# Kernel optimization log

Hardware: AMD Instinct MI355X
Metric: run time of the kernel (lower is better)

Reference implementation:

```python
import jax, jax.numpy as jnp
import numpy as np

B, N, D = 4, 2048, 2048
HEADS, KV_HEADS = 16, 4
DH = D // HEADS            # 128 per-head dim
KV_RATIO = HEADS // KV_HEADS
MAX_LEN, MAX_BSZ = 2048, 4
EPS = 1.1920929e-07        # torch.finfo(float32).eps (RMSNorm default eps=None)


def _rot_tables(n, d, base=10000.0):
    thetas = base ** (-jnp.arange(0, d, 2, dtype=jnp.float32) / d)   # [d/2]
    ang = jnp.arange(n, dtype=jnp.float32)[:, None] * thetas[None, :]
    cos = jnp.repeat(jnp.cos(ang), 2, axis=-1)   # [n, d] interleaved pairs
    sin = jnp.repeat(jnp.sin(ang), 2, axis=-1)
    return cos, sin


def _rotate_half_inverted(x):
    x1 = x[..., ::2]
    x2 = x[..., 1::2]
    return jnp.stack([-x2, x1], axis=-1).reshape(x.shape)


def _apply_rotation(x, end, start=0):
    cos, sin = _rot_tables(MAX_LEN, DH)
    return x * cos[start:end] + _rotate_half_inverted(x) * sin[start:end]


def setup_inputs() -> dict:
    key = jax.random.key(0)
    ks = jax.random.split(key, 4)
    s = 0.02
    return {
        "x": jax.random.normal(ks[0], (B, N, D), jnp.float32),
        "norm_w": jnp.ones((D,), jnp.float32),
        "qw": jax.random.normal(ks[1], (HEADS * DH, D), jnp.float32) * s,
        "qb": jnp.zeros((HEADS * DH,), jnp.float32),
        "kvw": jax.random.normal(ks[2], (2 * DH * KV_HEADS, D), jnp.float32) * s,
        "kvb": jnp.zeros((2 * DH * KV_HEADS,), jnp.float32),
        "wow": jax.random.normal(ks[3], (D, HEADS * DH), jnp.float32) * s,
        "wob": jnp.zeros((D,), jnp.float32),
        "kv_cache": jnp.zeros((MAX_BSZ, MAX_LEN, 2 * DH * KV_HEADS), jnp.float32),
        "pos": 0,
    }


def reference(x, norm_w, qw, qb, kvw, kvb, wow, wob, kv_cache, pos):
    b, n, d = x.shape
    t = pos + n  # total cached length
    # RMSNorm
    xn = x * jax.lax.rsqrt(jnp.mean(x * x, axis=-1, keepdims=True) + EPS) * norm_w
    # Q projection -> [b, heads, n, dh]
    q = (xn @ qw.T + qb).reshape(b, n, HEADS, DH).transpose(0, 2, 1, 3)
    # KV projection + cache write/read
    kv = xn @ kvw.T + kvb                                  # [b, n, 2*dh*kv_heads]
    cache = jax.lax.dynamic_update_slice(kv_cache, kv, (0, pos, 0))
    kvf = cache[:b, :t].reshape(b, t, KV_HEADS, 2 * DH).transpose(0, 2, 1, 3)
    kvf = jnp.repeat(kvf, KV_RATIO, axis=1)                # GQA expand -> [b, heads, t, 2dh]
    k, v = kvf[..., :DH], kvf[..., DH:]
    # RoPE (interleaved-pair variant)
    q = _apply_rotation(q, t, pos)
    k = _apply_rotation(k, t, 0)
    # Attention (decoder causal)
    attn = jnp.einsum("bhqd,bhkd->bhqk", q, k) / jnp.sqrt(jnp.float32(DH))
    if n > 1:
        mask = jnp.triu(jnp.ones((n, t), bool), k=1 + pos)
        attn = jnp.where(mask, -jnp.inf, attn)
    attn = jax.nn.softmax(attn, axis=-1)
    o = jnp.einsum("bhqk,bhkd->bhqd", attn, v).transpose(0, 2, 1, 3).reshape(b, n, HEADS * DH)
    return o @ wow.T + wob
```

## Files before the change

### kernel.cpp

```cpp
#include <hip/hip_runtime.h>
#include <hip/hip_bf16.h>

typedef unsigned short u16;
typedef unsigned int u32;
typedef __attribute__((ext_vector_type(4))) float f32x4;
typedef __attribute__((ext_vector_type(8))) short s16x8;

#define B_ 4
#define N_ 2048
#define D_ 2048
#define HEADS_ 16
#define KVH_ 4
#define DH_ 128
#define KVD_ 1024
#define M_ 8192
#define QSCALE2_ 0.12753257518622628f

__device__ __forceinline__ u16 f2bf(float f) {
  u32 u = __builtin_bit_cast(u32, f);
  return (u16)((u + 0x7FFFu + ((u >> 16) & 1u)) >> 16);
}

__device__ __forceinline__ float fexp2(float x) {
#if __has_builtin(__builtin_amdgcn_exp2f)
  return __builtin_amdgcn_exp2f(x);
#else
  return exp2f(x);
#endif
}

__device__ __forceinline__ void gload_lds16(const void* g, void* l) {
  __builtin_amdgcn_global_load_lds(
      (const __attribute__((address_space(1))) u32*)g,
      (__attribute__((address_space(3))) u32*)l, 16, 0, 0);
}

__global__ __launch_bounds__(256)
void rope_tab_k(float* __restrict__ cost, float* __restrict__ sint)
{
  const int idx = blockIdx.x * 256 + threadIdx.x;
  const int p = idx >> 6, i = idx & 63;
  const float theta = expf(-(float)i * 0.015625f * 9.210340371976184f);
  float s, c;
  sincosf((float)p * theta, &s, &c);
  cost[idx] = c;
  sint[idx] = s;
}

__global__ __launch_bounds__(256)
void cvt_bf16_k(const float* __restrict__ s, u16* __restrict__ d, int n)
{
  const int i = (blockIdx.x * 256 + threadIdx.x) * 8;
  if (i >= n) return;
  const f32x4 a = *(const f32x4*)(s + i);
  const f32x4 b = *(const f32x4*)(s + i + 4);
  s16x8 o;
  #pragma unroll
  for (int j = 0; j < 4; ++j) { o[j] = (short)f2bf(a[j]); o[4 + j] = (short)f2bf(b[j]); }
  *(s16x8*)(d + i) = o;
}

__global__ __launch_bounds__(256)
void rmsnorm_k(const float* __restrict__ x, const float* __restrict__ w, u16* __restrict__ xn)
{
  const int row = blockIdx.x, t = threadIdx.x;
  const float* xr = x + (size_t)row * D_;
  const f32x4 a = *(const f32x4*)(xr + t * 8);
  const f32x4 b = *(const f32x4*)(xr + t * 8 + 4);
  float ss = a[0]*a[0] + a[1]*a[1] + a[2]*a[2] + a[3]*a[3]
           + b[0]*b[0] + b[1]*b[1] + b[2]*b[2] + b[3]*b[3];
  #pragma unroll
  for (int off = 32; off >= 1; off >>= 1) ss += __shfl_xor(ss, off);
  __shared__ float wss[4];
  if ((t & 63) == 0) wss[t >> 6] = ss;
  __syncthreads();
  const float tot = wss[0] + wss[1] + wss[2] + wss[3];
  const float rs = rsqrtf(tot * (1.0f / D_) + 1.1920929e-07f);
  s16x8 o;
  #pragma unroll
  for (int j = 0; j < 4; ++j) {
    o[j]     = (short)f2bf(a[j] * rs * w[t * 8 + j]);
    o[4 + j] = (short)f2bf(b[j] * rs * w[t * 8 + 4 + j]);
  }
  *(s16x8*)(xn + (size_t)row * D_ + t * 8) = o;
}

template<int EPI>
__global__ __launch_bounds__(512, 2)
void gemm_p(const u16* __restrict__ A, const u16* __restrict__ Bw,
            void* __restrict__ Cv, void* __restrict__ Cv2,
            const float* __restrict__ bias, const float* __restrict__ bias2,
            const float* __restrict__ cos_t, const float* __restrict__ sin_t)
{
  __shared__ __align__(16) u16 As[2][8192];
  __shared__ __align__(16) u16 Bs[2][4096];
  const int t = threadIdx.x, w = t >> 6, l = t & 63;
  const int g = l >> 4, lr = l & 15;
  const int wm = w >> 2, wn = w & 3;

  const int nbx = gridDim.x;
  const int nb = nbx * gridDim.y;
  const int flat = blockIdx.y * nbx + blockIdx.x;
  const int swz = (flat & 7) * (nb >> 3) + (flat >> 3);
  const int row0 = (swz / nbx) * 256, col0 = (swz % nbx) * 128;

  const int NT = 64;

  const int srow = w * 16 + (l >> 2);
  const int scol = (l & 3) * 8;
  const u16* gA = A + (size_t)(row0 + srow) * 2048 + scol;
  const u16* gB = Bw + (size_t)(col0 + srow) * 2048 + scol;

  f32x4 acc[8][2] = {};

  auto stage_tile = [&](int kt2, int pb) {
    gload_lds16(gA + (size_t)kt2 * 32, &As[pb][(w * 16) * 32]);
    gload_lds16(gA + (size_t)128 * 2048 + kt2 * 32, &As[pb][(128 + w * 16) * 32]);
    gload_lds16(gB + (size_t)kt2 * 32, &Bs[pb][(w * 16) * 32]);
  };

  stage_tile(0, 0);

  for (int kt = 0; kt < NT; ++kt) {
    const int p = kt & 1;
    if (kt + 1 < NT) {
      stage_tile(kt + 1, p ^ 1);
      asm volatile("s_waitcnt vmcnt(3)" ::: "memory");
    } else {
      asm volatile("s_waitcnt vmcnt(0)" ::: "memory");
    }
    __builtin_amdgcn_s_barrier();

    s16x8 bf[2], af[8];
    #pragma unroll
    for (int nf = 0; nf < 2; ++nf)
      bf[nf] = *(const s16x8*)(&Bs[p][(wn * 32 + nf * 16 + lr) * 32 + g * 8]);
    #pragma unroll
    for (int mf = 0; mf < 8; ++mf)
      af[mf] = *(const s16x8*)(&As[p][(wm * 128 + mf * 16 + lr) * 32 + g * 8]);

    __builtin_amdgcn_s_setprio(1);
    #pragma unroll
    for (int mf = 0; mf < 8; ++mf)
      #pragma unroll
      for (int nf = 0; nf < 2; ++nf)
        acc[mf][nf] = __builtin_amdgcn_mfma_f32_16x16x32_bf16(af[mf], bf[nf], acc[mf][nf], 0, 0, 0);
    __builtin_amdgcn_s_setprio(0);
    __builtin_amdgcn_sched_barrier(0);
    __builtin_amdgcn_s_barrier();
  }

  #pragma unroll
  for (int mf = 0; mf < 8; ++mf) {
    #pragma unroll
    for (int nf = 0; nf < 2; ++nf) {
      const int cc = col0 + wn * 32 + nf * 16 + lr;
      const float bv = (EPI == 4 && cc >= 2048) ? bias2[cc - 2048] : bias[cc];
      #pragma unroll
      for (int j = 0; j < 4; ++j) {
        const int rr = row0 + wm * 128 + mf * 16 + g * 4 + j;
        float v = acc[mf][nf][j] + bv;
        if (EPI == 0) {
          ((float*)Cv)[(size_t)rr * 2048 + cc] = v;
        } else {
          const int pos = rr & (N_ - 1);
          const float pv = __shfl_xor(v, 1);
          if (cc < 2048) {
            const int d = cc & (DH_ - 1);
            const float c = cos_t[pos * 64 + (d >> 1)];
            const float s = sin_t[pos * 64 + (d >> 1)];
            const float o = (cc & 1) ? fmaf(v, c, pv * s) : fmaf(v, c, -pv * s);
            ((u16*)Cv)[(size_t)rr * 2048 + cc] = f2bf(o);
          } else {
            const int ccc = cc - 2048;
            const int dm = ccc & 255;
            float o = v;
            if (dm < DH_) {
              const float c = cos_t[pos * 64 + (dm >> 1)];
              const float s = sin_t[pos * 64 + (dm >> 1)];
              o = (dm & 1) ? fmaf(v, c, pv * s) : fmaf(v, c, -pv * s);
            }
            ((u16*)Cv2)[(size_t)rr * 1024 + ccc] = f2bf(o);
          }
        }
      }
    }
  }
}

__global__ __launch_bounds__(256)
void vtrans_k(const u16* __restrict__ kvb, u16* __restrict__ vt)
{
  __shared__ u16 tile[64][65];
  const int z = blockIdx.z, b = z >> 2, kh = z & 3;
  const int p0 = blockIdx.x * 64, d0 = blockIdx.y * 64;
  const int t = threadIdx.x;
  #pragma unroll
  for (int r = 0; r < 2; ++r) {
    const int pl = r * 32 + (t >> 3), dl = (t & 7) * 8;
    const s16x8 v = *(const s16x8*)(kvb + (size_t)(b * N_ + p0 + pl) * KVD_ + kh * 256 + 128 + d0 + dl);
    #pragma unroll
    for (int jj = 0; jj < 8; ++jj) tile[pl][dl + jj] = (u16)v[jj];
  }
  __syncthreads();
  #pragma unroll
  for (int r = 0; r < 2; ++r) {
    const int dl = r * 32 + (t >> 3), pl = (t & 7) * 8;
    s16x8 o;
    #pragma unroll
    for (int jj = 0; jj < 8; ++jj) o[jj] = (short)tile[pl + jj][dl];
    *(s16x8*)(vt + ((size_t)(z * DH_ + d0 + dl)) * N_ + p0 + pl) = o;
  }
}

__global__ __launch_bounds__(512, 2)
void attn_k(const u16* __restrict__ q, const u16* __restrict__ kvb,
            const u16* __restrict__ vt, u16* __restrict__ out)
{
  const int fi = blockIdx.x, h = blockIdx.y, b = blockIdx.z;
  const int kh = h >> 2;
  const int t = threadIdx.x, w = t >> 6, lane = t & 63;
  const int g = lane >> 4, lr = lane & 15;

  __shared__ __align__(16) u16 Ks[2][64 * 128];
  __shared__ __align__(16) u16 Vs[2][128 * 64];
  __shared__ __align__(16) u16 Ps[8][16 * 64];

  const int kc = 2 * w;
  const int kr0 = kc * 4 + (lane >> 4);
  const int ksw0 = (lane & 15) ^ (kr0 & 7);
  const int kr1 = kr0 + 4;
  const int ksw1 = (lane & 15) ^ (kr1 & 7);
  const int vd0 = kc * 8 + (lane >> 3);
  const int vsw0 = (lane & 7) ^ (vd0 & 7);
  const int vd1 = vd0 + 8;
  const int vsw1 = (lane & 7) ^ (vd1 & 7);

  const u16* kbase = kvb + (size_t)b * (N_ * KVD_) + kh * 256;
  const u16* vbase = vt + (size_t)((b * KVH_ + kh) * DH_) * N_;

  int cur = 0;

  auto issue = [&](int kt, int buf) {
    gload_lds16(kbase + (size_t)(kt * 64 + kr0) * KVD_ + ksw0 * 8, &Ks[buf][kc * 512]);
    gload_lds16(kbase + (size_t)(kt * 64 + kr1) * KVD_ + ksw1 * 8, &Ks[buf][(kc + 1) * 512]);
    gload_lds16(vbase + (size_t)vd0 * N_ + kt * 64 + vsw0 * 8, &Vs[buf][kc * 512]);
    gload_lds16(vbase + (size_t)vd1 * N_ + kt * 64 + vsw1 * 8, &Vs[buf][(kc + 1) * 512]);
  };

  auto run_qtile = [&](int qi, int nkt, bool chain) {
    const int qrow0 = qi * 128 + w * 16;
    const int td = qrow0 >> 6;
    s16x8 qf[4];
    {
      const u16* qp = q + (size_t)(b * N_ + qrow0 + lr) * D_ + h * DH_;
      #pragma unroll
      for (int ks = 0; ks < 4; ++ks) qf[ks] = *(const s16x8*)(qp + ks * 32 + g * 8);
    }
    f32x4 o_acc[8] = {};
    float m_j[4], l_j[4];
    #pragma unroll
    for (int j = 0; j < 4; ++j) { m_j[j] = -1e30f; l_j[j] = 0.0f; }

    for (int kt = 0; kt < nkt; ++kt) {
      __syncthreads();
      if (kt + 1 < nkt)      issue(kt + 1, cur ^ 1);
      else if (chain)        issue(0, cur ^ 1);

      if (kt <= td) {
        const u16* Kc = &Ks[cur][0];
        const u16* Vc = &Vs[cur][0];

        f32x4 sf[4] = {};
        __builtin_amdgcn_s_setprio(1);
        #pragma unroll
        for (int ks = 0; ks < 4; ++ks) {
          #pragma unroll
          for (int kvf = 0; kvf < 4; ++kvf) {
            const int kvr = kvf * 16 + lr;
            const int ba = (kvr * 256 + ks * 64 + g * 16) ^ ((kvr & 7) << 4);
            const s16x8 kf = *(const s16x8*)((const char*)Kc + ba);
            sf[kvf] = __builtin_amdgcn_mfma_f32_16x16x32_bf16(qf[ks], kf, sf[kvf], 0, 0, 0);
          }
        }
        __builtin_amdgcn_s_setprio(0);

        const bool need_mask = (kt == td);
        float pmax[4];
        #pragma unroll
        for (int j = 0; j < 4; ++j) {
          float mx = -1e30f;
          #pragma unroll
          for (int kvf = 0; kvf < 4; ++kvf) {
            float sv = sf[kvf][j] * QSCALE2_;
            if (need_mask) {
              const int kj = kt * 64 + kvf * 16 + lr;
              const int qi_row = qrow0 + g * 4 + j;
              if (kj > qi_row) sv = -1e30f;
            }
            sf[kvf][j] = sv;
            mx = fmaxf(mx, sv);
          }
          mx = fmaxf(mx, __shfl_xor(mx, 1));
          mx = fmaxf(mx, __shfl_xor(mx, 2));
          mx = fmaxf(mx, __shfl_xor(mx, 4));
          mx = fmaxf(mx, __shfl_xor(mx, 8));
          pmax[j] = mx;
        }

        const float needv = fmaxf(fmaxf(pmax[0] - m_j[0], pmax[1] - m_j[1]),
                                  fmaxf(pmax[2] - m_j[2], pmax[3] - m_j[3]));
        if (__any(needv > 8.0f)) {
          #pragma unroll
          for (int j = 0; j < 4; ++j) {
            const float mn = fmaxf(m_j[j], pmax[j]);
            const float pf = fexp2(m_j[j] - mn);
            m_j[j] = mn;
            l_j[j] *= pf;
            #pragma unroll
            for (int df = 0; df < 8; ++df) o_acc[df][j] *= pf;
          }
        }

        #pragma unroll
        for (int j = 0; j < 4; ++j) {
          float lacc = 0.0f;
          #pragma unroll
          for (int kvf = 0; kvf < 4; ++kvf) {
            const float p = fexp2(sf[kvf][j] - m_j[j]);
            lacc += p;
            const int rq = g * 4 + j, ck = kvf * 16 + lr;
            const int ba = (rq * 128 + ck * 2) ^ ((rq & 7) << 4);
            *(u16*)((char*)&Ps[w][0] + ba) = (u16)(__builtin_bit_cast(u32, p) >> 16);
          }
          l_j[j] += lacc;
        }

        __builtin_amdgcn_s_setprio(1);
        #pragma unroll
        for (int kk = 0; kk < 2; ++kk) {
          const int bap = (lr * 128 + kk * 64 + g * 16) ^ ((lr & 7) << 4);
          const s16x8 pf = *(const s16x8*)((const char*)&Ps[w][0] + bap);
          #pragma unroll
          for (int df = 0; df < 8; ++df) {
            const int dd = df * 16 + lr;
            const int bav = (dd * 128 + kk * 64 + g * 16) ^ ((dd & 7) << 4);
            const s16x8 vf = *(const s16x8*)((const char*)Vc + bav);
            o_acc[df] = __builtin_amdgcn_mfma_f32_16x16x32_bf16(pf, vf, o_acc[df], 0, 0, 0);
          }
        }
        __builtin_amdgcn_s_setprio(0);
      }
      cur ^= 1;
    }

    float inv_l[4];
    #pragma unroll
    for (int j = 0; j < 4; ++j) {
      float s4 = l_j[j];
      s4 += __shfl_xor(s4, 1);
      s4 += __shfl_xor(s4, 2);
      s4 += __shfl_xor(s4, 4);
      s4 += __shfl_xor(s4, 8);
      inv_l[j] = 1.0f / s4;
    }
    u16* op = out + (size_t)(b * N_ + qrow0) * D_ + h * DH_;
    #pragma unroll
    for (int df = 0; df < 8; ++df)
      #pragma unroll
      for (int j = 0; j < 4; ++j)
        op[(size_t)(g * 4 + j) * D_ + df * 16 + lr] = f2bf(o_acc[df][j] * inv_l[j]);
  };

  const int qlo = fi, qhi = 15 - fi;
  issue(0, 0);
  run_qtile(qlo, 2 * qlo + 2, true);
  run_qtile(qhi, 2 * qhi + 2, false);
}

extern "C" void kernel_launch(void* const* d_in, const int* in_sizes, int n_in,
                              void* d_out, int out_size, void* d_ws, size_t ws_size,
                              hipStream_t stream) {
  const float* x      = (const float*)d_in[0];
  const float* normw  = (const float*)d_in[1];
  const float* qw     = (const float*)d_in[2];
  const float* qbias  = (const float*)d_in[3];
  const float* kvw    = (const float*)d_in[4];
  const float* kvbias = (const float*)d_in[5];
  const float* wow    = (const float*)d_in[6];
  const float* wob    = (const float*)d_in[7];
  float* out = (float*)d_out;

  char* ws = (char*)d_ws;
  u16* xn    = (u16*)(ws + 0);
  u16* dq    = (u16*)(ws + 33554432);
  u16* dkv   = (u16*)(ws + 67108864);
  u16* dvt   = (u16*)(ws + 83886080);
  u16* wqkv  = (u16*)(ws + 92274688);
  u16* wowb  = (u16*)(ws + 104857600);
  float* cost = (float*)(ws + 113246208);
  float* sint = (float*)(ws + 113770496);

  rope_tab_k<<<512, 256, 0, stream>>>(cost, sint);
  cvt_bf16_k<<<2048, 256, 0, stream>>>(qw, wqkv, 2048 * 2048);
  cvt_bf16_k<<<1024, 256, 0, stream>>>(kvw, wqkv + 2048 * 2048, 1024 * 2048);
  cvt_bf16_k<<<2048, 256, 0, stream>>>(wow, wowb, 2048 * 2048);
  rmsnorm_k<<<8192, 256, 0, stream>>>(x, normw, xn);
  gemm_p<4><<<dim3(24, 32), 512, 0, stream>>>(xn, wqkv, (void*)dq, (void*)dkv,
                                              qbias, kvbias, cost, sint);
  vtrans_k<<<dim3(32, 2, 16), 256, 0, stream>>>(dkv, dvt);
  attn_k<<<dim3(8, 16, 4), 512, 0, stream>>>(dq, dkv, dvt, xn);
  gemm_p<0><<<dim3(16, 32), 512, 0, stream>>>(xn, wowb, (void*)out, nullptr,
                                              wob, nullptr, nullptr, nullptr);
}
```

Measured before the change: 423.1 us.

## Single-buffer V tile, reload Q per tile, and add Ps swizzle bit

V is now loaded into a single LDS buffer within the same iteration rather than double-buffered ahead, with an explicit vmcnt wait before the PV MFMA. The goal is to cut LDS use and let more blocks fit per CU. Q fragments are re-read from global memory each live iteration instead of being held in registers for the whole tile, which lowers register pressure. The P-tile swizzle gains a higher XOR bit to reduce LDS bank conflicts. In exchange, V load latency is exposed within each iteration and Q is reloaded repeatedly.

```diff
diff --git a/kernel.cpp b/kernel.cpp
--- a/kernel.cpp
+++ b/kernel.cpp
@@ -223,40 +223,36 @@
   const int g = lane >> 4, lr = lane & 15;
 
   __shared__ __align__(16) u16 Ks[2][64 * 128];
-  __shared__ __align__(16) u16 Vs[2][128 * 64];
+  __shared__ __align__(16) u16 Vs[128 * 64];
   __shared__ __align__(16) u16 Ps[8][16 * 64];
-
-  const int kc = 2 * w;
-  const int kr0 = kc * 4 + (lane >> 4);
-  const int ksw0 = (lane & 15) ^ (kr0 & 7);
-  const int kr1 = kr0 + 4;
-  const int ksw1 = (lane & 15) ^ (kr1 & 7);
-  const int vd0 = kc * 8 + (lane >> 3);
-  const int vsw0 = (lane & 7) ^ (vd0 & 7);
-  const int vd1 = vd0 + 8;
-  const int vsw1 = (lane & 7) ^ (vd1 & 7);
 
   const u16* kbase = kvb + (size_t)b * (N_ * KVD_) + kh * 256;
   const u16* vbase = vt + (size_t)((b * KVH_ + kh) * DH_) * N_;
 
-  int cur = 0;
-
-  auto issue = [&](int kt, int buf) {
+  auto issueK = [&](int kt, int buf) {
+    const int kc = 2 * w;
+    const int kr0 = kc * 4 + (lane >> 4);
+    const int ksw0 = (lane & 15) ^ (kr0 & 7);
+    const int kr1 = kr0 + 4;
+    const int ksw1 = (lane & 15) ^ (kr1 & 7);
     gload_lds16(kbase + (size_t)(kt * 64 + kr0) * KVD_ + ksw0 * 8, &Ks[buf][kc * 512]);
     gload_lds16(kbase + (size_t)(kt * 64 + kr1) * KVD_ + ksw1 * 8, &Ks[buf][(kc + 1) * 512]);
-    gload_lds16(vbase + (size_t)vd0 * N_ + kt * 64 + vsw0 * 8, &Vs[buf][kc * 512]);
-    gload_lds16(vbase + (size_t)vd1 * N_ + kt * 64 + vsw1 * 8, &Vs[buf][(kc + 1) * 512]);
   };
+  auto issueV = [&](int kt) {
+    const int kc = 2 * w;
+    const int vd0 = kc * 8 + (lane >> 3);
+    const int vsw0 = (lane & 7) ^ (vd0 & 7);
+    const int vd1 = vd0 + 8;
+    const int vsw1 = (lane & 7) ^ (vd1 & 7);
+    gload_lds16(vbase + (size_t)vd0 * N_ + kt * 64 + vsw0 * 8, &Vs[kc * 512]);
+    gload_lds16(vbase + (size_t)vd1 * N_ + kt * 64 + vsw1 * 8, &Vs[(kc + 1) * 512]);
+  };
+
+  int cur = 0;
 
   auto run_qtile = [&](int qi, int nkt, bool chain) {
     const int qrow0 = qi * 128 + w * 16;
     const int td = qrow0 >> 6;
-    s16x8 qf[4];
-    {
-      const u16* qp = q + (size_t)(b * N_ + qrow0 + lr) * D_ + h * DH_;
-      #pragma unroll
-      for (int ks = 0; ks < 4; ++ks) qf[ks] = *(const s16x8*)(qp + ks * 32 + g * 8);
-    }
     f32x4 o_acc[8] = {};
     float m_j[4], l_j[4];
     #pragma unroll
@@ -264,12 +260,22 @@
 
     for (int kt = 0; kt < nkt; ++kt) {
       __syncthreads();
-      if (kt + 1 < nkt)      issue(kt + 1, cur ^ 1);
-      else if (chain)        issue(0, cur ^ 1);
-
-      if (kt <= td) {
+      const bool live = (kt <= td);
+      const bool havek = (kt + 1 < nkt) || chain;
+
+      s16x8 qf[4];
+      if (live) {
+        int zoff; asm volatile("s_mov_b32 %0, 0" : "=s"(zoff));
+        const u16* qp = q + (size_t)(b * N_ + qrow0 + lr) * D_ + h * DH_ + zoff;
+        #pragma unroll
+        for (int ks = 0; ks < 4; ++ks) qf[ks] = *(const s16x8*)(qp + ks * 32 + g * 8);
+      }
+      issueV(kt);
+      if (kt + 1 < nkt)      issueK(kt + 1, cur ^ 1);
+      else if (chain)        issueK(0, cur ^ 1);
+
+      if (live) {
         const u16* Kc = &Ks[cur][0];
-        const u16* Vc = &Vs[cur][0];
 
         f32x4 sf[4] = {};
         __builtin_amdgcn_s_setprio(1);
@@ -330,22 +336,25 @@
             const float p = fexp2(sf[kvf][j] - m_j[j]);
             lacc += p;
             const int rq = g * 4 + j, ck = kvf * 16 + lr;
-            const int ba = (rq * 128 + ck * 2) ^ ((rq & 7) << 4);
+            const int ba = rq * 128 + ((ck * 2) ^ ((rq & 7) << 4) ^ ((rq & 8) << 2));
             *(u16*)((char*)&Ps[w][0] + ba) = (u16)(__builtin_bit_cast(u32, p) >> 16);
           }
           l_j[j] += lacc;
         }
+
+        if (havek) asm volatile("s_waitcnt vmcnt(2)" ::: "memory");
+        else       asm volatile("s_waitcnt vmcnt(0)" ::: "memory");
 
         __builtin_amdgcn_s_setprio(1);
         #pragma unroll
         for (int kk = 0; kk < 2; ++kk) {
-          const int bap = (lr * 128 + kk * 64 + g * 16) ^ ((lr & 7) << 4);
+          const int bap = lr * 128 + ((kk * 64 + g * 16) ^ ((lr & 7) << 4) ^ ((lr & 8) << 2));
           const s16x8 pf = *(const s16x8*)((const char*)&Ps[w][0] + bap);
           #pragma unroll
           for (int df = 0; df < 8; ++df) {
             const int dd = df * 16 + lr;
             const int bav = (dd * 128 + kk * 64 + g * 16) ^ ((dd & 7) << 4);
-            const s16x8 vf = *(const s16x8*)((const char*)Vc + bav);
+            const s16x8 vf = *(const s16x8*)((const char*)Vs + bav);
             o_acc[df] = __builtin_amdgcn_mfma_f32_16x16x32_bf16(pf, vf, o_acc[df], 0, 0, 0);
           }
         }
@@ -373,7 +382,7 @@
   };
 
   const int qlo = fi, qhi = 15 - fi;
-  issue(0, 0);
+  issueK(0, 0);
   run_qtile(qlo, 2 * qlo + 2, true);
   run_qtile(qhi, 2 * qhi + 2, false);
 }
```

After: 453.3 us. +7.2%, slower.

## Shrink attention tiles to 64 query rows and 32-key blocks, drop paired tiles

Applied to the files above, without the earlier changes.

The attention kernel now uses 256-thread blocks, each covering one 64-row query tile, with 32-key K/V tiles. It replaces the old scheme where each 512-thread block processed a paired light and heavy 128-row tile. Blocks are launched heaviest-first (qi = 31 - blockIdx.x) to balance the causal load, and the K/V swizzles and P buffer padding are redone for the smaller tiles. This means more, smaller blocks and less LDS per block, so occupancy should rise. In exchange, each loaded K/V tile is reused by fewer queries and there are more barrier iterations per unit of work.

```diff
diff --git a/kernel.cpp b/kernel.cpp
--- a/kernel.cpp
+++ b/kernel.cpp
@@ -213,169 +213,156 @@
   }
 }
 
-__global__ __launch_bounds__(512, 2)
+__global__ __launch_bounds__(256, 3)
 void attn_k(const u16* __restrict__ q, const u16* __restrict__ kvb,
             const u16* __restrict__ vt, u16* __restrict__ out)
 {
-  const int fi = blockIdx.x, h = blockIdx.y, b = blockIdx.z;
+  const int qi = 31 - blockIdx.x, h = blockIdx.y, b = blockIdx.z;
   const int kh = h >> 2;
   const int t = threadIdx.x, w = t >> 6, lane = t & 63;
   const int g = lane >> 4, lr = lane & 15;
 
-  __shared__ __align__(16) u16 Ks[2][64 * 128];
-  __shared__ __align__(16) u16 Vs[2][128 * 64];
-  __shared__ __align__(16) u16 Ps[8][16 * 64];
-
-  const int kc = 2 * w;
-  const int kr0 = kc * 4 + (lane >> 4);
-  const int ksw0 = (lane & 15) ^ (kr0 & 7);
-  const int kr1 = kr0 + 4;
-  const int ksw1 = (lane & 15) ^ (kr1 & 7);
-  const int vd0 = kc * 8 + (lane >> 3);
-  const int vsw0 = (lane & 7) ^ (vd0 & 7);
-  const int vd1 = vd0 + 8;
-  const int vsw1 = (lane & 7) ^ (vd1 & 7);
+  __shared__ __align__(16) u16 Ks[2][32 * 128];
+  __shared__ __align__(16) u16 Vs[2][128 * 32];
+  __shared__ __align__(16) u16 Ps[4][16 * 40];
 
   const u16* kbase = kvb + (size_t)b * (N_ * KVD_) + kh * 256;
   const u16* vbase = vt + (size_t)((b * KVH_ + kh) * DH_) * N_;
 
+  auto issue = [&](int kt, int buf) {
+    #pragma unroll
+    for (int i = 0; i < 2; ++i) {
+      const int c = 2 * w + i;
+      const int kr = 4 * c + (lane >> 4);
+      const int ksw = (lane & 15) ^ (kr & 15);
+      gload_lds16(kbase + (size_t)(kt * 32 + kr) * KVD_ + ksw * 8, &Ks[buf][c * 512]);
+      const int vr = 16 * c + (lane >> 2);
+      const int vsw = (lane & 3) ^ (vr & 3);
+      gload_lds16(vbase + (size_t)vr * N_ + kt * 32 + vsw * 8, &Vs[buf][c * 512]);
+    }
+  };
+
+  const int qrow0 = qi * 64 + w * 16;
+  const int td = (qrow0 + 15) >> 5;
+  const int nkt = 2 * qi + 2;
+
+  s16x8 qf[4];
+  {
+    const u16* qp = q + (size_t)(b * N_ + qrow0 + lr) * D_ + h * DH_;
+    #pragma unroll
+    for (int ks = 0; ks < 4; ++ks) qf[ks] = *(const s16x8*)(qp + ks * 32 + g * 8);
+  }
+  f32x4 o_acc[8] = {};
+  float m_j[4], l_j[4];
+  #pragma unroll
+  for (int j = 0; j < 4; ++j) { m_j[j] = -1e30f; l_j[j] = 0.0f; }
+
+  issue(0, 0);
   int cur = 0;
 
-  auto issue = [&](int kt, int buf) {
-    gload_lds16(kbase + (size_t)(kt * 64 + kr0) * KVD_ + ksw0 * 8, &Ks[buf][kc * 512]);
-    gload_lds16(kbase + (size_t)(kt * 64 + kr1) * KVD_ + ksw1 * 8, &Ks[buf][(kc + 1) * 512]);
-    gload_lds16(vbase + (size_t)vd0 * N_ + kt * 64 + vsw0 * 8, &Vs[buf][kc * 512]);
-    gload_lds16(vbase + (size_t)vd1 * N_ + kt * 64 + vsw1 * 8, &Vs[buf][(kc + 1) * 512]);
-  };
-
-  auto run_qtile = [&](int qi, int nkt, bool chain) {
-    const int qrow0 = qi * 128 + w * 16;
-    const int td = qrow0 >> 6;
-    s16x8 qf[4];
-    {
-      const u16* qp = q + (size_t)(b * N_ + qrow0 + lr) * D_ + h * DH_;
-      #pragma unroll
-      for (int ks = 0; ks < 4; ++ks) qf[ks] = *(const s16x8*)(qp + ks * 32 + g * 8);
-    }
-    f32x4 o_acc[8] = {};
-    float m_j[4], l_j[4];
-    #pragma unroll
-    for (int j = 0; j < 4; ++j) { m_j[j] = -1e30f; l_j[j] = 0.0f; }
-
-    for (int kt = 0; kt < nkt; ++kt) {
-      __syncthreads();
-      if (kt + 1 < nkt)      issue(kt + 1, cur ^ 1);
-      else if (chain)        issue(0, cur ^ 1);
-
-      if (kt <= td) {
-        const u16* Kc = &Ks[cur][0];
-        const u16* Vc = &Vs[cur][0];
-
-        f32x4 sf[4] = {};
-        __builtin_amdgcn_s_setprio(1);
+  for (int kt = 0; kt < nkt; ++kt) {
+    __syncthreads();
+    if (kt + 1 < nkt) issue(kt + 1, cur ^ 1);
+
+    if (kt <= td) {
+      const u16* Kc = &Ks[cur][0];
+      const u16* Vc = &Vs[cur][0];
+
+      f32x4 sf[2] = {};
+      __builtin_amdgcn_s_setprio(1);
+      #pragma unroll
+      for (int ks = 0; ks < 4; ++ks) {
         #pragma unroll
-        for (int ks = 0; ks < 4; ++ks) {
-          #pragma unroll
-          for (int kvf = 0; kvf < 4; ++kvf) {
-            const int kvr = kvf * 16 + lr;
-            const int ba = (kvr * 256 + ks * 64 + g * 16) ^ ((kvr & 7) << 4);
-            const s16x8 kf = *(const s16x8*)((const char*)Kc + ba);
-            sf[kvf] = __builtin_amdgcn_mfma_f32_16x16x32_bf16(qf[ks], kf, sf[kvf], 0, 0, 0);
+        for (int kvf = 0; kvf < 2; ++kvf) {
+          const int kvr = kvf * 16 + lr;
+          const int ba = kvr * 256 + ((ks * 64 + g * 16) ^ ((kvr & 15) << 4));
+          const s16x8 kf = *(const s16x8*)((const char*)Kc + ba);
+          sf[kvf] = __builtin_amdgcn_mfma_f32_16x16x32_bf16(qf[ks], kf, sf[kvf], 0, 0, 0);
+        }
+      }
+      __builtin_amdgcn_s_setprio(0);
+
+      const bool need_mask = (kt == td);
+      float pmax[4];
+      #pragma unroll
+      for (int j = 0; j < 4; ++j) {
+        float mx = -1e30f;
+        #pragma unroll
+        for (int kvf = 0; kvf < 2; ++kvf) {
+          float sv = sf[kvf][j] * QSCALE2_;
+          if (need_mask) {
+            const int kj = kt * 32 + kvf * 16 + lr;
+            const int qi_row = qrow0 + g * 4 + j;
+            if (kj > qi_row) sv = -1e30f;
           }
+          sf[kvf][j] = sv;
+          mx = fmaxf(mx, sv);
         }
-        __builtin_amdgcn_s_setprio(0);
-
-        const bool need_mask = (kt == td);
-        float pmax[4];
+        mx = fmaxf(mx, __shfl_xor(mx, 1));
+        mx = fmaxf(mx, __shfl_xor(mx, 2));
+        mx = fmaxf(mx, __shfl_xor(mx, 4));
+        mx = fmaxf(mx, __shfl_xor(mx, 8));
+        pmax[j] = mx;
+      }
+
+      const float needv = fmaxf(fmaxf(pmax[0] - m_j[0], pmax[1] - m_j[1]),
+                                fmaxf(pmax[2] - m_j[2], pmax[3] - m_j[3]));
+      if (__any(needv > 8.0f)) {
         #pragma unroll
         for (int j = 0; j < 4; ++j) {
-          float mx = -1e30f;
+          const float mn = fmaxf(m_j[j], pmax[j]);
+          const float pf = fexp2(m_j[j] - mn);
+          m_j[j] = mn;
+          l_j[j] *= pf;
           #pragma unroll
-          for (int kvf = 0; kvf < 4; ++kvf) {
-            float sv = sf[kvf][j] * QSCALE2_;
-            if (need_mask) {
-              const int kj = kt * 64 + kvf * 16 + lr;
-              const int qi_row = qrow0 + g * 4 + j;
-              if (kj > qi_row) sv = -1e30f;
-            }
-            sf[kvf][j] = sv;
-            mx = fmaxf(mx, sv);
-          }
-          mx = fmaxf(mx, __shfl_xor(mx, 1));
-          mx = fmaxf(mx, __shfl_xor(mx, 2));
-          mx = fmaxf(mx, __shfl_xor(mx, 4));
-          mx = fmaxf(mx, __shfl_xor(mx, 8));
-          pmax[j] = mx;
+          for (int df = 0; df < 8; ++df) o_acc[df][j] *= pf;
         }
-
-        const float needv = fmaxf(fmaxf(pmax[0] - m_j[0], pmax[1] - m_j[1]),
-                                  fmaxf(pmax[2] - m_j[2], pmax[3] - m_j[3]));
-        if (__any(needv > 8.0f)) {
-          #pragma unroll
-          for (int j = 0; j < 4; ++j) {
-            const float mn = fmaxf(m_j[j], pmax[j]);
-            const float pf = fexp2(m_j[j] - mn);
-            m_j[j] = mn;
-            l_j[j] *= pf;
-            #pragma unroll
-            for (int df = 0; df < 8; ++df) o_acc[df][j] *= pf;
-          }
+      }
+
+      #pragma unroll
+      for (int j = 0; j < 4; ++j) {
+        float lacc = 0.0f;
+        #pragma unroll
+        for (int kvf = 0; kvf < 2; ++kvf) {
+          const float p = fexp2(sf[kvf][j] - m_j[j]);
+          lacc += p;
+          const int rq = g * 4 + j, ck = kvf * 16 + lr;
+          *(u16*)((char*)&Ps[w][0] + rq * 80 + ck * 2) =
+              (u16)(__builtin_bit_cast(u32, p) >> 16);
         }
-
-        #pragma unroll
-        for (int j = 0; j < 4; ++j) {
-          float lacc = 0.0f;
-          #pragma unroll
-          for (int kvf = 0; kvf < 4; ++kvf) {
-            const float p = fexp2(sf[kvf][j] - m_j[j]);
-            lacc += p;
-            const int rq = g * 4 + j, ck = kvf * 16 + lr;
-            const int ba = (rq * 128 + ck * 2) ^ ((rq & 7) << 4);
-            *(u16*)((char*)&Ps[w][0] + ba) = (u16)(__builtin_bit_cast(u32, p) >> 16);
-          }
-          l_j[j] += lacc;
-        }
-
-        __builtin_amdgcn_s_setprio(1);
-        #pragma unroll
-        for (int kk = 0; kk < 2; ++kk) {
-          const int bap = (lr * 128 + kk * 64 + g * 16) ^ ((lr & 7) << 4);
-          const s16x8 pf = *(const s16x8*)((const char*)&Ps[w][0] + bap);
-          #pragma unroll
-          for (int df = 0; df < 8; ++df) {
-            const int dd = df * 16 + lr;
-            const int bav = (dd * 128 + kk * 64 + g * 16) ^ ((dd & 7) << 4);
-            const s16x8 vf = *(const s16x8*)((const char*)Vc + bav);
-            o_acc[df] = __builtin_amdgcn_mfma_f32_16x16x32_bf16(pf, vf, o_acc[df], 0, 0, 0);
-          }
-        }
-        __builtin_amdgcn_s_setprio(0);
-      }
-      cur ^= 1;
+        l_j[j] += lacc;
+      }
+
+      const s16x8 pf = *(const s16x8*)((const char*)&Ps[w][0] + lr * 80 + g * 16);
+      __builtin_amdgcn_s_setprio(1);
+      #pragma unroll
+      for (int df = 0; df < 8; ++df) {
+        const int dd = df * 16 + lr;
+        const int bav = dd * 64 + ((g * 16) ^ ((dd & 3) << 4));
+        const s16x8 vf = *(const s16x8*)((const char*)Vc + bav);
+        o_acc[df] = __builtin_amdgcn_mfma_f32_16x16x32_bf16(pf, vf, o_acc[df], 0, 0, 0);
+      }
+      __builtin_amdgcn_s_setprio(0);
     }
-
-    float inv_l[4];
-    #pragma unroll
-    for (int j = 0; j < 4; ++j) {
-      float s4 = l_j[j];
-      s4 += __shfl_xor(s4, 1);
-      s4 += __shfl_xor(s4, 2);
-      s4 += __shfl_xor(s4, 4);
-      s4 += __shfl_xor(s4, 8);
-      inv_l[j] = 1.0f / s4;
-    }
-    u16* op = out + (size_t)(b * N_ + qrow0) * D_ + h * DH_;
-    #pragma unroll
-    for (int df = 0; df < 8; ++df)
-      #pragma unroll
-      for (int j = 0; j < 4; ++j)
-        op[(size_t)(g * 4 + j) * D_ + df * 16 + lr] = f2bf(o_acc[df][j] * inv_l[j]);
-  };
-
-  const int qlo = fi, qhi = 15 - fi;
-  issue(0, 0);
-  run_qtile(qlo, 2 * qlo + 2, true);
-  run_qtile(qhi, 2 * qhi + 2, false);
+    cur ^= 1;
+  }
+
+  float inv_l[4];
+  #pragma unroll
+  for (int j = 0; j < 4; ++j) {
+    float s4 = l_j[j];
+    s4 += __shfl_xor(s4, 1);
+    s4 += __shfl_xor(s4, 2);
+    s4 += __shfl_xor(s4, 4);
+    s4 += __shfl_xor(s4, 8);
+    inv_l[j] = 1.0f / s4;
+  }
+  u16* op = out + (size_t)(b * N_ + qrow0) * D_ + h * DH_;
+  #pragma unroll
+  for (int df = 0; df < 8; ++df)
+    #pragma unroll
+    for (int j = 0; j < 4; ++j)
+      op[(size_t)(g * 4 + j) * D_ + df * 16 + lr] = f2bf(o_acc[df][j] * inv_l[j]);
 }
 
 extern "C" void kernel_launch(void* const* d_in, const int* in_sizes, int n_in,
@@ -409,7 +396,7 @@
   gemm_p<4><<<dim3(24, 32), 512, 0, stream>>>(xn, wqkv, (void*)dq, (void*)dkv,
                                               qbias, kvbias, cost, sint);
   vtrans_k<<<dim3(32, 2, 16), 256, 0, stream>>>(dkv, dvt);
-  attn_k<<<dim3(8, 16, 4), 512, 0, stream>>>(dq, dkv, dvt, xn);
+  attn_k<<<dim3(32, 16, 4), 256, 0, stream>>>(dq, dkv, dvt, xn);
   gemm_p<0><<<dim3(16, 32), 512, 0, stream>>>(xn, wowb, (void*)out, nullptr,
                                               wob, nullptr, nullptr, nullptr);
 }
```

Result: slower. 538.3 us (+27.2%).

## Triple-buffer K/V tiles in attention with a single fused loop over both q-tiles

Applied to the files above, without the earlier changes.

Replaces the double-buffered K/V LDS staging with a three-stage ring, issuing loads two tiles ahead and waiting with explicit vmcnt counts before each barrier. The two per-block q-tiles are merged into one flat loop, so the prefetch continues across the tile boundary. The point is to hide more global-load latency behind MFMA work. In exchange LDS use rises, and launch bounds drop to one block per CU, which lowers occupancy.

```diff
diff --git a/kernel.cpp b/kernel.cpp
--- a/kernel.cpp
+++ b/kernel.cpp
@@ -213,7 +213,7 @@
   }
 }
 
-__global__ __launch_bounds__(512, 2)
+__global__ __launch_bounds__(512, 1)
 void attn_k(const u16* __restrict__ q, const u16* __restrict__ kvb,
             const u16* __restrict__ vt, u16* __restrict__ out)
 {
@@ -222,8 +222,8 @@
   const int t = threadIdx.x, w = t >> 6, lane = t & 63;
   const int g = lane >> 4, lr = lane & 15;
 
-  __shared__ __align__(16) u16 Ks[2][64 * 128];
-  __shared__ __align__(16) u16 Vs[2][128 * 64];
+  __shared__ __align__(16) u16 Ks[3][64 * 128];
+  __shared__ __align__(16) u16 Vs[3][128 * 64];
   __shared__ __align__(16) u16 Ps[8][16 * 64];
 
   const int kc = 2 * w;
@@ -239,8 +239,6 @@
   const u16* kbase = kvb + (size_t)b * (N_ * KVD_) + kh * 256;
   const u16* vbase = vt + (size_t)((b * KVH_ + kh) * DH_) * N_;
 
-  int cur = 0;
-
   auto issue = [&](int kt, int buf) {
     gload_lds16(kbase + (size_t)(kt * 64 + kr0) * KVD_ + ksw0 * 8, &Ks[buf][kc * 512]);
     gload_lds16(kbase + (size_t)(kt * 64 + kr1) * KVD_ + ksw1 * 8, &Ks[buf][(kc + 1) * 512]);
@@ -248,112 +246,25 @@
     gload_lds16(vbase + (size_t)vd1 * N_ + kt * 64 + vsw1 * 8, &Vs[buf][(kc + 1) * 512]);
   };
 
-  auto run_qtile = [&](int qi, int nkt, bool chain) {
-    const int qrow0 = qi * 128 + w * 16;
-    const int td = qrow0 >> 6;
-    s16x8 qf[4];
-    {
-      const u16* qp = q + (size_t)(b * N_ + qrow0 + lr) * D_ + h * DH_;
-      #pragma unroll
-      for (int ks = 0; ks < 4; ++ks) qf[ks] = *(const s16x8*)(qp + ks * 32 + g * 8);
-    }
-    f32x4 o_acc[8] = {};
-    float m_j[4], l_j[4];
-    #pragma unroll
-    for (int j = 0; j < 4; ++j) { m_j[j] = -1e30f; l_j[j] = 0.0f; }
-
-    for (int kt = 0; kt < nkt; ++kt) {
-      __syncthreads();
-      if (kt + 1 < nkt)      issue(kt + 1, cur ^ 1);
-      else if (chain)        issue(0, cur ^ 1);
-
-      if (kt <= td) {
-        const u16* Kc = &Ks[cur][0];
-        const u16* Vc = &Vs[cur][0];
-
-        f32x4 sf[4] = {};
-        __builtin_amdgcn_s_setprio(1);
-        #pragma unroll
-        for (int ks = 0; ks < 4; ++ks) {
-          #pragma unroll
-          for (int kvf = 0; kvf < 4; ++kvf) {
-            const int kvr = kvf * 16 + lr;
-            const int ba = (kvr * 256 + ks * 64 + g * 16) ^ ((kvr & 7) << 4);
-            const s16x8 kf = *(const s16x8*)((const char*)Kc + ba);
-            sf[kvf] = __builtin_amdgcn_mfma_f32_16x16x32_bf16(qf[ks], kf, sf[kvf], 0, 0, 0);
-          }
-        }
-        __builtin_amdgcn_s_setprio(0);
-
-        const bool need_mask = (kt == td);
-        float pmax[4];
-        #pragma unroll
-        for (int j = 0; j < 4; ++j) {
-          float mx = -1e30f;
-          #pragma unroll
-          for (int kvf = 0; kvf < 4; ++kvf) {
-            float sv = sf[kvf][j] * QSCALE2_;
-            if (need_mask) {
-              const int kj = kt * 64 + kvf * 16 + lr;
-              const int qi_row = qrow0 + g * 4 + j;
-              if (kj > qi_row) sv = -1e30f;
-            }
-            sf[kvf][j] = sv;
-            mx = fmaxf(mx, sv);
-          }
-          mx = fmaxf(mx, __shfl_xor(mx, 1));
-          mx = fmaxf(mx, __shfl_xor(mx, 2));
-          mx = fmaxf(mx, __shfl_xor(mx, 4));
-          mx = fmaxf(mx, __shfl_xor(mx, 8));
-          pmax[j] = mx;
-        }
-
-        const float needv = fmaxf(fmaxf(pmax[0] - m_j[0], pmax[1] - m_j[1]),
-                                  fmaxf(pmax[2] - m_j[2], pmax[3] - m_j[3]));
-        if (__any(needv > 8.0f)) {
-          #pragma unroll
-          for (int j = 0; j < 4; ++j) {
-            const float mn = fmaxf(m_j[j], pmax[j]);
-            const float pf = fexp2(m_j[j] - mn);
-            m_j[j] = mn;
-            l_j[j] *= pf;
-            #pragma unroll
-            for (int df = 0; df < 8; ++df) o_acc[df][j] *= pf;
-          }
-        }
-
-        #pragma unroll
-        for (int j = 0; j < 4; ++j) {
-          float lacc = 0.0f;
-          #pragma unroll
-          for (int kvf = 0; kvf < 4; ++kvf) {
-            const float p = fexp2(sf[kvf][j] - m_j[j]);
-            lacc += p;
-            const int rq = g * 4 + j, ck = kvf * 16 + lr;
-            const int ba = (rq * 128 + ck * 2) ^ ((rq & 7) << 4);
-            *(u16*)((char*)&Ps[w][0] + ba) = (u16)(__builtin_bit_cast(u32, p) >> 16);
-          }
-          l_j[j] += lacc;
-        }
-
-        __builtin_amdgcn_s_setprio(1);
-        #pragma unroll
-        for (int kk = 0; kk < 2; ++kk) {
-          const int bap = (lr * 128 + kk * 64 + g * 16) ^ ((lr & 7) << 4);
-          const s16x8 pf = *(const s16x8*)((const char*)&Ps[w][0] + bap);
-          #pragma unroll
-          for (int df = 0; df < 8; ++df) {
-            const int dd = df * 16 + lr;
-            const int bav = (dd * 128 + kk * 64 + g * 16) ^ ((dd & 7) << 4);
-            const s16x8 vf = *(const s16x8*)((const char*)Vc + bav);
-            o_acc[df] = __builtin_amdgcn_mfma_f32_16x16x32_bf16(pf, vf, o_acc[df], 0, 0, 0);
-          }
-        }
-        __builtin_amdgcn_s_setprio(0);
-      }
-      cur ^= 1;
-    }
-
+  const int qlo = fi, qhi = 15 - fi;
+  const int nkt0 = 2 * qlo + 2;
+  const int ntot = nkt0 + 2 * qhi + 2;
+
+  int qrow0 = qlo * 128 + w * 16;
+  int td = qrow0 >> 6;
+
+  s16x8 qf[4];
+  {
+    const u16* qp = q + (size_t)(b * N_ + qrow0 + lr) * D_ + h * DH_;
+    #pragma unroll
+    for (int ks = 0; ks < 4; ++ks) qf[ks] = *(const s16x8*)(qp + ks * 32 + g * 8);
+  }
+  f32x4 o_acc[8] = {};
+  float m_j[4], l_j[4];
+  #pragma unroll
+  for (int j = 0; j < 4; ++j) { m_j[j] = -1e30f; l_j[j] = 0.0f; }
+
+  auto store_out = [&]() {
     float inv_l[4];
     #pragma unroll
     for (int j = 0; j < 4; ++j) {
@@ -372,10 +283,121 @@
         op[(size_t)(g * 4 + j) * D_ + df * 16 + lr] = f2bf(o_acc[df][j] * inv_l[j]);
   };
 
-  const int qlo = fi, qhi = 15 - fi;
   issue(0, 0);
-  run_qtile(qlo, 2 * qlo + 2, true);
-  run_qtile(qhi, 2 * qhi + 2, false);
+  issue(1, 1);
+
+  for (int v = 0; v < ntot; ++v) {
+    if (v + 1 < ntot) asm volatile("s_waitcnt vmcnt(4)" ::: "memory");
+    else              asm volatile("s_waitcnt vmcnt(0)" ::: "memory");
+    __builtin_amdgcn_s_barrier();
+
+    if (v + 2 < ntot) {
+      const int v2 = v + 2;
+      issue(v2 < nkt0 ? v2 : v2 - nkt0, v2 % 3);
+    }
+
+    if (v == nkt0) {
+      store_out();
+      qrow0 = qhi * 128 + w * 16;
+      td = qrow0 >> 6;
+      const u16* qp = q + (size_t)(b * N_ + qrow0 + lr) * D_ + h * DH_;
+      #pragma unroll
+      for (int ks = 0; ks < 4; ++ks) qf[ks] = *(const s16x8*)(qp + ks * 32 + g * 8);
+      #pragma unroll
+      for (int df = 0; df < 8; ++df) o_acc[df] = (f32x4){0.f, 0.f, 0.f, 0.f};
+      #pragma unroll
+      for (int j = 0; j < 4; ++j) { m_j[j] = -1e30f; l_j[j] = 0.0f; }
+    }
+
+    const int kt = (v < nkt0) ? v : v - nkt0;
+    if (kt <= td) {
+      const int cb = v % 3;
+      const u16* Kc = &Ks[cb][0];
+      const u16* Vc = &Vs[cb][0];
+
+      f32x4 sf[4] = {};
+      __builtin_amdgcn_s_setprio(1);
+      #pragma unroll
+      for (int ks = 0; ks < 4; ++ks) {
+        #pragma unroll
+        for (int kvf = 0; kvf < 4; ++kvf) {
+          const int kvr = kvf * 16 + lr;
+          const int ba = (kvr * 256 + ks * 64 + g * 16) ^ ((kvr & 7) << 4);
+          const s16x8 kf = *(const s16x8*)((const char*)Kc + ba);
+          sf[kvf] = __builtin_amdgcn_mfma_f32_16x16x32_bf16(qf[ks], kf, sf[kvf], 0, 0, 0);
+        }
+      }
+      __builtin_amdgcn_s_setprio(0);
+
+      const bool need_mask = (kt == td);
+      float pmax[4];
+      #pragma unroll
+      for (int j = 0; j < 4; ++j) {
+        float mx = -1e30f;
+        #pragma unroll
+        for (int kvf = 0; kvf < 4; ++kvf) {
+          float sv = sf[kvf][j] * QSCALE2_;
+          if (need_mask) {
+            const int kj = kt * 64 + kvf * 16 + lr;
+            const int qi_row = qrow0 + g * 4 + j;
+            if (kj > qi_row) sv = -1e30f;
+          }
+          sf[kvf][j] = sv;
+          mx = fmaxf(mx, sv);
+        }
+        mx = fmaxf(mx, __shfl_xor(mx, 1));
+        mx = fmaxf(mx, __shfl_xor(mx, 2));
+        mx = fmaxf(mx, __shfl_xor(mx, 4));
+        mx = fmaxf(mx, __shfl_xor(mx, 8));
+        pmax[j] = mx;
+      }
+
+      const float needv = fmaxf(fmaxf(pmax[0] - m_j[0], pmax[1] - m_j[1]),
+                                fmaxf(pmax[2] - m_j[2], pmax[3] - m_j[3]));
+      if (__any(needv > 8.0f)) {
+        #pragma unroll
+        for (int j = 0; j < 4; ++j) {
+          const float mn = fmaxf(m_j[j], pmax[j]);
+          const float pf = fexp2(m_j[j] - mn);
+          m_j[j] = mn;
+          l_j[j] *= pf;
+          #pragma unroll
+          for (int df = 0; df < 8; ++df) o_acc[df][j] *= pf;
+        }
+      }
+
+      #pragma unroll
+      for (int j = 0; j < 4; ++j) {
+        float lacc = 0.0f;
+        #pragma unroll
+        for (int kvf = 0; kvf < 4; ++kvf) {
+          const float p = fexp2(sf[kvf][j] - m_j[j]);
+          lacc += p;
+          const int rq = g * 4 + j, ck = kvf * 16 + lr;
+          const int ba = (rq * 128 + ck * 2) ^ ((rq & 7) << 4);
+          *(u16*)((char*)&Ps[w][0] + ba) = (u16)(__builtin_bit_cast(u32, p) >> 16);
+        }
+        l_j[j] += lacc;
+      }
+
+      __builtin_amdgcn_s_setprio(1);
+      #pragma unroll
+      for (int kk = 0; kk < 2; ++kk) {
+        const int bap = (lr * 128 + kk * 64 + g * 16) ^ ((lr & 7) << 4);
+        const s16x8 pf = *(const s16x8*)((const char*)&Ps[w][0] + bap);
+        #pragma unroll
+        for (int df = 0; df < 8; ++df) {
+          const int dd = df * 16 + lr;
+          const int bav = (dd * 128 + kk * 64 + g * 16) ^ ((dd & 7) << 4);
+          const s16x8 vf = *(const s16x8*)((const char*)Vc + bav);
+          o_acc[df] = __builtin_amdgcn_mfma_f32_16x16x32_bf16(pf, vf, o_acc[df], 0, 0, 0);
+        }
+      }
+      __builtin_amdgcn_s_setprio(0);
+    }
+  }
+
+  store_out();
 }
 
 extern "C" void kernel_launch(void* const* d_in, const int* in_sizes, int n_in,
```

Result: slower. 433.9 us (+2.6%).
